# Kernel tuning notes

Measured on AMD Instinct MI355X. Metric: run time of the kernel, lower is better.

## Reference

```python
import jax, jax.numpy as jnp
import numpy as np

B, S, HID, H, D = 2, 2048, 2048, 16, 128
ROPE_THETA = 10000.0
NEG = -1e9


def _rope_tables(seq_len, dim, theta):
    inv_freq = 1.0 / (theta ** (jnp.arange(0, dim, 2, dtype=jnp.float32) / dim))
    t = jnp.arange(seq_len, dtype=jnp.float32)
    freqs = jnp.outer(t, inv_freq)                 # [S, D/2]
    emb = jnp.concatenate([freqs, freqs], axis=-1)  # [S, D]
    return jnp.cos(emb), jnp.sin(emb)


def _rotate_half(x):
    x1, x2 = jnp.split(x, 2, axis=-1)
    return jnp.concatenate([-x2, x1], axis=-1)


def setup_inputs() -> dict:
    key = jax.random.key(0)
    ks = jax.random.split(key, 12)
    hidden_states = jax.random.normal(ks[0], (B, S, HID), dtype=jnp.float32)
    Wq = jax.random.normal(ks[1], (HID, HID), dtype=jnp.float32) * 0.02
    Wk = jax.random.normal(ks[2], (HID, HID), dtype=jnp.float32) * 0.02
    Wv = jax.random.normal(ks[3], (HID, HID), dtype=jnp.float32) * 0.02
    Wo = jax.random.normal(ks[4], (HID, HID), dtype=jnp.float32) * 0.02
    bq = jnp.zeros((HID,), jnp.float32)
    bk = jnp.zeros((HID,), jnp.float32)
    bv = jnp.zeros((HID,), jnp.float32)
    beta = jax.random.normal(ks[5], (1,), dtype=jnp.float32)
    M = jax.random.normal(ks[6], (H, D, D), dtype=jnp.float32) * 0.01
    z = jax.random.uniform(ks[7], (H, D), dtype=jnp.float32) + 1.0  # strictly positive normalizer
    causal = jnp.tril(jnp.ones((S, S), dtype=bool))
    attention_mask = jnp.broadcast_to(
        jnp.where(causal, 0.0, NEG).astype(jnp.float32)[None, None], (B, 1, S, S)
    ) + jnp.zeros((B, 1, S, S), jnp.float32)
    position_ids = jnp.broadcast_to(jnp.arange(S, dtype=jnp.int32), (B, S))
    return {
        "hidden_states": hidden_states, "Wq": Wq, "bq": bq, "Wk": Wk, "bk": bk,
        "Wv": Wv, "bv": bv, "Wo": Wo, "beta": beta, "M": M, "z": z,
        "attention_mask": attention_mask, "position_ids": position_ids,
    }


def reference(hidden_states, Wq, bq, Wk, bk, Wv, bv, Wo, beta, M, z,
              attention_mask, position_ids):
    bsz, seq, hid = hidden_states.shape
    h, d = M.shape[0], M.shape[1]

    # projections (weights stored [in, out])
    q = (hidden_states @ Wq + bq).reshape(bsz, seq, h, d).transpose(0, 2, 1, 3)  # [b,h,s,d]
    k = (hidden_states @ Wk + bk).reshape(bsz, seq, h, d).transpose(0, 2, 1, 3)
    v = (hidden_states @ Wv + bv).reshape(bsz, seq, h, d).transpose(0, 2, 1, 3)

    # RoPE
    cos, sin = _rope_tables(seq, d, ROPE_THETA)          # [s, d]
    cos = cos[position_ids][:, None]                      # [b,1,s,d]
    sin = sin[position_ids][:, None]
    q = q * cos + _rotate_half(q) * sin
    k = k * cos + _rotate_half(k) * sin

    sigma = lambda x: jax.nn.elu(x) + 1.0
    sig_q = sigma(q)
    sig_k = sigma(k)

    # compressive-memory retrieval (uses pre-update M, z)
    mem_num = jnp.einsum('bhsd,hde->bhse', sig_q, M)
    mem_den = jnp.einsum('bhsd,hd->bhs', sig_q, z)
    memory_output = mem_num / mem_den[..., None]

    # memory update via outer products of feature-mapped keys and values
    M_new = M + jnp.einsum('bhsd,bhse->hde', sig_k, v)
    z_new = z + sig_k.sum(axis=(0, 2))

    # local causal attention
    scores = jnp.einsum('bhqd,bhkd->bhqk', q, k) / jnp.sqrt(jnp.float32(d))
    scores = scores + attention_mask
    attn = jax.nn.softmax(scores, axis=-1)
    attn_output = jnp.einsum('bhqk,bhkd->bhqd', attn, v)

    # gated long-term injection
    g = jax.nn.sigmoid(beta)[0]
    combined = g * memory_output + (1.0 - g) * attn_output

    combined = combined.transpose(0, 2, 1, 3).reshape(bsz, seq, h * d)
    final_output = combined @ Wo
    return (final_output, M_new, z_new)
```

## Files before the change

### kernel.cpp

```cpp
#include <hip/hip_runtime.h>


typedef float  floatx4 __attribute__((ext_vector_type(4)));
typedef __bf16 bf16x8  __attribute__((ext_vector_type(8)));

#define DEV __device__ __forceinline__

constexpr int BN  = 2;
constexpr int SS  = 2048;
constexpr int HID = 2048;
constexpr int NH  = 16;
constexpr int DD  = 128;
constexpr int BS  = BN * SS;

DEV unsigned short f2bf(float f) {
  unsigned int u = __float_as_uint(f);
  u += 0x7FFFu + ((u >> 16) & 1u);
  return (unsigned short)(u >> 16);
}
DEV float bf2f(unsigned short h) {
  return __uint_as_float(((unsigned int)h) << 16);
}
DEV float sigma_f(float x) { return x > 0.f ? x + 1.f : __expf(x); }

DEV void cp16(const unsigned short* g, unsigned short* l) {
  __builtin_amdgcn_global_load_lds(
      (const __attribute__((address_space(1))) unsigned int*)g,
      (__attribute__((address_space(3))) unsigned int*)l, 16, 0, 0);
}

DEV bf16x8 scale8(bf16x8 x, float s) {
  bf16x8 r;
  #pragma unroll
  for (int i = 0; i < 8; i++) r[i] = (__bf16)((float)x[i] * s);
  return r;
}

constexpr size_t WS_WOT   = 0;
constexpr size_t WS_HSB   = WS_WOT   + (size_t)HID * HID * 2;
constexpr size_t WS_WQT   = WS_HSB   + (size_t)BS  * HID * 2;
constexpr size_t WS_WKT   = WS_WQT   + (size_t)HID * HID * 2;
constexpr size_t WS_WVT   = WS_WKT   + (size_t)HID * HID * 2;
constexpr size_t WS_QB    = WS_WVT   + (size_t)HID * HID * 2;
constexpr size_t WS_KB    = WS_QB    + (size_t)BS  * HID * 2;
constexpr size_t WS_VB    = WS_KB    + (size_t)BS  * HID * 2;
constexpr size_t WS_VTB   = WS_VB    + (size_t)BS  * HID * 2;
constexpr size_t WS_ATT   = WS_VTB   + (size_t)BS  * HID * 2;
constexpr size_t WS_COMB  = WS_ATT   + (size_t)BS  * HID * 2;
constexpr size_t WS_MPART = WS_COMB  + (size_t)BS  * HID * 2;
constexpr size_t WS_ZPART = WS_MPART + (size_t)16 * NH * DD * DD * 4;

__global__ __launch_bounds__(256) void k_prep(const float* __restrict__ hs,
                                              const float* __restrict__ Wq, const float* __restrict__ Wk,
                                              const float* __restrict__ Wv, const float* __restrict__ Wo,
                                              unsigned short* __restrict__ hsb,
                                              unsigned short* tq, unsigned short* tk,
                                              unsigned short* tv, unsigned short* to_) {
  __shared__ float tile[64][65];
  const int tid = threadIdx.x;
  if (blockIdx.z == 4) {
    int cid = blockIdx.y * 32 + blockIdx.x;
    const float4* src = (const float4*)hs;
    ushort4* dst = (ushort4*)hsb;
    #pragma unroll
    for (int i = 0; i < 8; i++) {
      int idx = cid * 2048 + i * 256 + tid;
      float4 v = src[idx];
      ushort4 o; o.x = f2bf(v.x); o.y = f2bf(v.y); o.z = f2bf(v.z); o.w = f2bf(v.w);
      dst[idx] = o;
    }
    return;
  }
  const float* W; unsigned short* T;
  switch (blockIdx.z) {
    case 0:  W = Wq; T = tq; break;
    case 1:  W = Wk; T = tk; break;
    case 2:  W = Wv; T = tv; break;
    default: W = Wo; T = to_; break;
  }
  int k0 = blockIdx.y * 64, n0 = blockIdx.x * 64;
  #pragma unroll
  for (int i = 0; i < 16; i++) {
    int idx = i * 256 + tid; int r = idx >> 6, c = idx & 63;
    tile[r][c] = W[(size_t)(k0 + r) * HID + n0 + c];
  }
  __syncthreads();
  #pragma unroll
  for (int i = 0; i < 16; i++) {
    int idx = i * 256 + tid; int r = idx >> 6, c = idx & 63;
    T[(size_t)(n0 + r) * HID + k0 + c] = f2bf(tile[c][r]);
  }
}

constexpr int GBM = 256, GBN = 128, GBK = 64;
constexpr int NTK = HID / GBK;
constexpr int SLOT_U = (GBM + GBN) * GBK;
constexpr int A_U    = GBM * GBK;

DEV void stage_tile(const unsigned short* __restrict__ X,
                    const unsigned short* __restrict__ Wt,
                    unsigned short* slot, int m0, int n0, int k0, int tid) {
  #pragma unroll
  for (int i = 0; i < 4; i++) {
    int c = i * 512 + tid;
    int row = c >> 3;
    int col = k0 + (((c & 7) ^ (row & 7)) << 3);
    cp16(X + (size_t)(m0 + row) * HID + col, slot + c * 8);
  }
  #pragma unroll
  for (int i = 0; i < 2; i++) {
    int c = i * 512 + tid;
    int row = c >> 3;
    int col = k0 + (((c & 7) ^ (row & 7)) << 3);
    cp16(Wt + (size_t)(n0 + row) * HID + col, slot + A_U + c * 8);
  }
}

DEV void gemm_core(const unsigned short* __restrict__ X,
                   const unsigned short* __restrict__ Wt,
                   unsigned short* lds, int m0, int n0, floatx4 acc[4][4]) {
  const int tid = threadIdx.x;
  const int lane = tid & 63, w = tid >> 6;
  const int grp = lane >> 4, l16 = lane & 15;
  const int wm = (w >> 1) * 64, wn = (w & 1) * 64;
  const int swz = (l16 & 7) << 3;
  #pragma unroll
  for (int i = 0; i < 4; i++)
    #pragma unroll
    for (int j = 0; j < 4; j++) acc[i][j] = floatx4{0.f, 0.f, 0.f, 0.f};
  stage_tile(X, Wt, lds,          m0, n0, 0,   tid);
  stage_tile(X, Wt, lds + SLOT_U, m0, n0, GBK, tid);
  int sl_r = 0, sl_w = 2;
  for (int t = 0; t < NTK; t++) {
    if (t + 1 < NTK) asm volatile("s_waitcnt vmcnt(6)" ::: "memory");
    else             asm volatile("s_waitcnt vmcnt(0)" ::: "memory");
    __builtin_amdgcn_s_barrier();
    asm volatile("" ::: "memory");
    if (t + 2 < NTK)
      stage_tile(X, Wt, lds + sl_w * SLOT_U, m0, n0, (t + 2) * GBK, tid);
    const unsigned short* As = lds + sl_r * SLOT_U;
    const unsigned short* Bs = As + A_U;
    bf16x8 af[4][2], bfr[4][2];
    #pragma unroll
    for (int mi = 0; mi < 4; mi++)
      #pragma unroll
      for (int ks = 0; ks < 2; ks++)
        af[mi][ks] = __builtin_bit_cast(bf16x8,
            *(const uint4*)(As + (wm + mi * 16 + l16) * 64 + ((ks * 32 + grp * 8) ^ swz)));
    #pragma unroll
    for (int ni = 0; ni < 4; ni++)
      #pragma unroll
      for (int ks = 0; ks < 2; ks++)
        bfr[ni][ks] = __builtin_bit_cast(bf16x8,
            *(const uint4*)(Bs + (wn + ni * 16 + l16) * 64 + ((ks * 32 + grp * 8) ^ swz)));
    __builtin_amdgcn_s_setprio(1);
    #pragma unroll
    for (int mi = 0; mi < 4; mi++)
      #pragma unroll
      for (int ni = 0; ni < 4; ni++)
        #pragma unroll
        for (int ks = 0; ks < 2; ks++)
          acc[mi][ni] = __builtin_amdgcn_mfma_f32_16x16x32_bf16(af[mi][ks], bfr[ni][ks], acc[mi][ni], 0, 0, 0);
    __builtin_amdgcn_s_setprio(0);
    asm volatile("" ::: "memory");
    sl_r = (sl_r == 2) ? 0 : sl_r + 1;
    sl_w = (sl_w == 2) ? 0 : sl_w + 1;
  }
}

__global__ __launch_bounds__(512, 2) void k_gemm_qkv(
    const unsigned short* __restrict__ Xb,
    const unsigned short* __restrict__ Wtq, const unsigned short* __restrict__ Wtk,
    const unsigned short* __restrict__ Wtv,
    const float* __restrict__ bq, const float* __restrict__ bk, const float* __restrict__ bv,
    unsigned short* __restrict__ qb, unsigned short* __restrict__ kb,
    unsigned short* __restrict__ vb, unsigned short* __restrict__ vtb) {
  const unsigned short* Wt; const float* bias; unsigned short* out;
  switch (blockIdx.z) {
    case 0:  Wt = Wtq; bias = bq; out = qb; break;
    case 1:  Wt = Wtk; bias = bk; out = kb; break;
    default: Wt = Wtv; bias = bv; out = vb; break;
  }
  __shared__ __align__(16) unsigned short lds[3 * SLOT_U];
  int lin = blockIdx.y * 16 + blockIdx.x;
  lin = (lin & 7) * 32 + (lin >> 3);
  int m0 = (lin >> 4) * GBM, n0 = (lin & 15) * GBN;
  floatx4 acc[4][4];
  gemm_core(Xb, Wt, lds, m0, n0, acc);
  const int lane = threadIdx.x & 63, w = threadIdx.x >> 6;
  const int grp = lane >> 4, l16 = lane & 15;
  const int wm = (w >> 1) * 64, wn = (w & 1) * 64;
  const bool isv = (blockIdx.z == 2);
  #pragma unroll
  for (int mi = 0; mi < 4; mi++) {
    int gr0 = m0 + wm + mi * 16;
    int bi  = gr0 >> 11;
    int ssb = (gr0 & 2047) + grp * 4;
    #pragma unroll
    for (int ni = 0; ni < 4; ni++) {
      int col = n0 + wn + ni * 16 + l16;
      float bb_ = bias[col];
      int hh = col >> 7, dd = col & 127;
      ushort4 pk;
      unsigned short* pv = (unsigned short*)&pk;
      #pragma unroll
      for (int r = 0; r < 4; r++) {
        unsigned short val = f2bf(acc[mi][ni][r] + bb_);
        out[(((size_t)(bi * NH + hh)) * SS + ssb + r) * DD + dd] = val;
        pv[r] = val;
      }
      if (isv)
        *(ushort4*)(vtb + (((size_t)(bi * NH + hh)) * DD + dd) * SS + ssb) = pk;
    }
  }
}

__global__ __launch_bounds__(512, 2) void k_gemm_out(const unsigned short* __restrict__ Xb,
                                                     const unsigned short* __restrict__ Wt,
                                                     float* __restrict__ outf) {
  __shared__ __align__(16) unsigned short lds[3 * SLOT_U];
  int lin = blockIdx.y * 16 + blockIdx.x;
  lin = (lin & 7) * 32 + (lin >> 3);
  int m0 = (lin >> 4) * GBM, n0 = (lin & 15) * GBN;
  floatx4 acc[4][4];
  gemm_core(Xb, Wt, lds, m0, n0, acc);
  const int lane = threadIdx.x & 63, w = threadIdx.x >> 6;
  const int grp = lane >> 4, l16 = lane & 15;
  const int wm = (w >> 1) * 64, wn = (w & 1) * 64;
  #pragma unroll
  for (int mi = 0; mi < 4; mi++)
    #pragma unroll
    for (int ni = 0; ni < 4; ni++) {
      int col = n0 + wn + ni * 16 + l16;
      #pragma unroll
      for (int r = 0; r < 4; r++) {
        int gr = m0 + wm + mi * 16 + grp * 4 + r;
        outf[(size_t)gr * HID + col] = acc[mi][ni][r];
      }
    }
}

__global__ __launch_bounds__(256) void k_rope(unsigned short* __restrict__ qb,
                                              unsigned short* __restrict__ kb) {
  int row = blockIdx.x * 4 + (threadIdx.x >> 6);
  int d = threadIdx.x & 63;
  int s = row & (SS - 1);
  size_t base = (size_t)row * DD;
  float ang = (float)s * __expf(-(float)d * (9.210340371976184f / 64.f));
  float sn, c;
  __sincosf(ang, &sn, &c);
  float q1 = bf2f(qb[base + d]), q2 = bf2f(qb[base + d + 64]);
  qb[base + d]      = f2bf(q1 * c - q2 * sn);
  qb[base + d + 64] = f2bf(q2 * c + q1 * sn);
  float k1 = bf2f(kb[base + d]), k2 = bf2f(kb[base + d + 64]);
  kb[base + d]      = f2bf(k1 * c - k2 * sn);
  kb[base + d + 64] = f2bf(k2 * c + k1 * sn);
}

DEV void stage_kv(const unsigned short* __restrict__ Kg,
                  const unsigned short* __restrict__ Vg,
                  unsigned short* Klb, unsigned short* Vtlb, int tid) {
  #pragma unroll
  for (int i = 0; i < 4; i++) {
    int c = i * 256 + tid;
    int kv = c >> 4, ck = c & 15;
    cp16(Kg + kv * DD + ((ck ^ (kv & 7)) << 3), Klb + c * 8);
    int dvt = c >> 3, cv = c & 7;
    cp16(Vg + (size_t)dvt * SS + ((cv ^ (dvt & 7)) << 3), Vtlb + c * 8);
  }
}

DEV void attn_update(const unsigned short* Kl, const unsigned short* Vtl,
                     unsigned short* Plw, const bf16x8* qf, floatx4* o,
                     floatx4* lacc, bool diag, int grp, int l16, int wrow) {
  const int swk = l16 & 7;
  floatx4 sacc[4];
  #pragma unroll
  for (int j = 0; j < 4; j++) sacc[j] = floatx4{0.f, 0.f, 0.f, 0.f};
  __builtin_amdgcn_s_setprio(1);
  #pragma unroll
  for (int ks = 0; ks < 4; ks++)
    #pragma unroll
    for (int j = 0; j < 4; j++) {
      bf16x8 kf = __builtin_bit_cast(bf16x8,
          *(const uint4*)(Kl + (j * 16 + l16) * 128 + (((ks * 4 + grp) ^ swk) << 3)));
      sacc[j] = __builtin_amdgcn_mfma_f32_16x16x32_bf16(qf[ks], kf, sacc[j], 0, 0, 0);
    }
  __builtin_amdgcn_s_setprio(0);
  #pragma unroll
  for (int j = 0; j < 4; j++)
    #pragma unroll
    for (int r = 0; r < 4; r++) {
      float p = (diag && (j * 16 + l16) > (wrow + grp * 4 + r)) ? 0.f : __expf(sacc[j][r]);
      Plw[(j >> 1) * 640 + (grp * 4 + r) * 40 + (j & 1) * 16 + l16] = f2bf(p);
    }
  const bf16x8 ones = __builtin_bit_cast(bf16x8,
      uint4{0x3F803F80u, 0x3F803F80u, 0x3F803F80u, 0x3F803F80u});
  __builtin_amdgcn_s_setprio(1);
  #pragma unroll
  for (int ks2 = 0; ks2 < 2; ks2++) {
    bf16x8 pf = __builtin_bit_cast(bf16x8,
        *(const uint4*)(Plw + ks2 * 640 + l16 * 40 + grp * 8));
    *lacc = __builtin_amdgcn_mfma_f32_16x16x32_bf16(pf, ones, *lacc, 0, 0, 0);
    #pragma unroll
    for (int n = 0; n < 8; n++) {
      bf16x8 vf = __builtin_bit_cast(bf16x8,
          *(const uint4*)(Vtl + (n * 16 + l16) * 64 + (((ks2 * 4 + grp) ^ swk) << 3)));
      o[n] = __builtin_amdgcn_mfma_f32_16x16x32_bf16(pf, vf, o[n], 0, 0, 0);
    }
  }
  __builtin_amdgcn_s_setprio(0);
}

__global__ __launch_bounds__(256) void k_attn(const unsigned short* __restrict__ qb,
                                              const unsigned short* __restrict__ kb,
                                              const unsigned short* __restrict__ vtb,
                                              unsigned short* __restrict__ attb) {
  const int t = blockIdx.x, bh = blockIdx.y;
  const int qtA = t, qtB = 31 - t;
  const int tid = threadIdx.x, w = tid >> 6, lane = tid & 63;
  const int grp = lane >> 4, l16 = lane & 15;
  const unsigned short* Q  = qb  + (size_t)bh * SS * DD;
  const unsigned short* K  = kb  + (size_t)bh * SS * DD;
  const unsigned short* VT = vtb + (size_t)bh * DD * SS;
  __shared__ __align__(16) unsigned short Kl[2][64 * 128];
  __shared__ __align__(16) unsigned short Vtl[2][128 * 64];
  __shared__ __align__(16) unsigned short Pl[4][1280];
  const float sc = 0.08838834764831845f;
  bf16x8 qfA[4], qfB[4];
  {
    int qrA = qtA * 64 + w * 16 + l16, qrB = qtB * 64 + w * 16 + l16;
    #pragma unroll
    for (int ks = 0; ks < 4; ks++) {
      qfA[ks] = scale8(__builtin_bit_cast(bf16x8, *(const uint4*)(Q + (size_t)qrA * DD + ks * 32 + grp * 8)), sc);
      qfB[ks] = scale8(__builtin_bit_cast(bf16x8, *(const uint4*)(Q + (size_t)qrB * DD + ks * 32 + grp * 8)), sc);
    }
  }
  floatx4 oA[8], oB[8];
  #pragma unroll
  for (int n = 0; n < 8; n++) { oA[n] = floatx4{0,0,0,0}; oB[n] = floatx4{0,0,0,0}; }
  floatx4 laccA = floatx4{0,0,0,0}, laccB = floatx4{0,0,0,0};
  stage_kv(K, VT, Kl[0], Vtl[0], tid);
  asm volatile("s_waitcnt vmcnt(0)" ::: "memory");
  __builtin_amdgcn_s_barrier();
  int cur = 0;
  for (int kt = 0; kt <= qtB; kt++) {
    asm volatile("" ::: "memory");
    if (kt < qtB)
      stage_kv(K + (size_t)(kt + 1) * 64 * DD, VT + (size_t)(kt + 1) * 64,
               Kl[cur ^ 1], Vtl[cur ^ 1], tid);
    attn_update(Kl[cur], Vtl[cur], Pl[w], qfB, oB, &laccB, kt == qtB, grp, l16, w * 16);
    if (kt <= qtA)
      attn_update(Kl[cur], Vtl[cur], Pl[w], qfA, oA, &laccA, kt == qtA, grp, l16, w * 16);
    asm volatile("" ::: "memory");
    if (kt < qtB) {
      asm volatile("s_waitcnt vmcnt(0)" ::: "memory");
      __builtin_amdgcn_s_barrier();
    }
    cur ^= 1;
  }
  #pragma unroll
  for (int r = 0; r < 4; r++) {
    float invA = 1.f / laccA[r], invB = 1.f / laccB[r];
    int rA = qtA * 64 + w * 16 + grp * 4 + r;
    int rB = qtB * 64 + w * 16 + grp * 4 + r;
    #pragma unroll
    for (int n = 0; n < 8; n++) {
      attb[(size_t)bh * SS * DD + (size_t)rA * DD + n * 16 + l16] = f2bf(oA[n][r] * invA);
      attb[(size_t)bh * SS * DD + (size_t)rB * DD + n * 16 + l16] = f2bf(oB[n][r] * invB);
    }
  }
}

__global__ __launch_bounds__(256) void k_memcomb(const unsigned short* __restrict__ qb,
                                                 const float* __restrict__ M,
                                                 const float* __restrict__ z,
                                                 const float* __restrict__ beta,
                                                 const unsigned short* __restrict__ attb,
                                                 unsigned short* __restrict__ comb) {
  const int st = blockIdx.x, bh = blockIdx.y;
  const int b = bh >> 4, h = bh & 15;
  const int tid = threadIdx.x;
  const int te = tid & 31, ts = tid >> 5;
  const int s0 = st * 64;
  __shared__ float Ml[16][128];
  __shared__ float sq[64][16];
  __shared__ float zl[16];
  float acc[8][4]; float den[8];
  #pragma unroll
  for (int i = 0; i < 8; i++) { den[i] = 0.f; for (int j = 0; j < 4; j++) acc[i][j] = 0.f; }
  const float* Mh = M + (size_t)h * DD * DD;
  for (int dc = 0; dc < DD; dc += 16) {
    __syncthreads();
    #pragma unroll
    for (int i = 0; i < 8; i++) {
      int idx = i * 256 + tid; int r = idx >> 7, cc = idx & 127;
      Ml[r][cc] = Mh[(size_t)(dc + r) * DD + cc];
    }
    #pragma unroll
    for (int i = 0; i < 4; i++) {
      int idx = i * 256 + tid; int r = idx >> 4, cc = idx & 15;
      sq[r][cc] = sigma_f(bf2f(qb[((size_t)bh * SS + s0 + r) * DD + dc + cc]));
    }
    if (tid < 16) zl[tid] = z[h * DD + dc + tid];
    __syncthreads();
    for (int dd = 0; dd < 16; dd++) {
      float zv = zl[dd];
      float m0_ = Ml[dd][te * 4 + 0], m1_ = Ml[dd][te * 4 + 1];
      float m2_ = Ml[dd][te * 4 + 2], m3_ = Ml[dd][te * 4 + 3];
      #pragma unroll
      for (int si = 0; si < 8; si++) {
        float sv = sq[ts * 8 + si][dd];
        den[si] += sv * zv;
        acc[si][0] += sv * m0_; acc[si][1] += sv * m1_;
        acc[si][2] += sv * m2_; acc[si][3] += sv * m3_;
      }
    }
  }
  float g = 1.f / (1.f + __expf(-beta[0]));
  #pragma unroll
  for (int si = 0; si < 8; si++) {
    int s = s0 + ts * 8 + si;
    float dinv = 1.f / den[si];
    #pragma unroll
    for (int ei = 0; ei < 4; ei++) {
      float mo = acc[si][ei] * dinv;
      float at = bf2f(attb[((size_t)bh * SS + s) * DD + te * 4 + ei]);
      float cvv = g * mo + (1.f - g) * at;
      comb[((size_t)(b * SS + s)) * HID + h * DD + te * 4 + ei] = f2bf(cvv);
    }
  }
}

__global__ __launch_bounds__(256) void k_mnew(const unsigned short* __restrict__ kb,
                                              const unsigned short* __restrict__ vb,
                                              float* __restrict__ mpart,
                                              float* __restrict__ zpart) {
  const int ch = blockIdx.x, h = blockIdx.y;
  const int tid = threadIdx.x;
  const int td = tid >> 4, te = tid & 15;
  __shared__ float sk[16][128], vv[16][128];
  float acc[8][8];
  float zacc = 0.f;
  #pragma unroll
  for (int a = 0; a < 8; a++)
    #pragma unroll
    for (int b2 = 0; b2 < 8; b2++) acc[a][b2] = 0.f;
  for (int c0 = 0; c0 < 256; c0 += 16) {
    __syncthreads();
    #pragma unroll
    for (int i = 0; i < 8; i++) {
      int idx = i * 256 + tid; int r = idx >> 7, cc = idx & 127;
      int bs = ch * 256 + c0 + r;
      size_t addr = ((size_t)((bs >> 11) * NH + h) * SS + (bs & 2047)) * DD + cc;
      float skv = sigma_f(bf2f(kb[addr]));
      sk[r][cc] = skv;
      zacc += skv;
      vv[r][cc] = bf2f(vb[addr]);
    }
    __syncthreads();
    for (int i = 0; i < 16; i++) {
      float ks_[8], vs_[8];
      #pragma unroll
      for (int a = 0; a < 8; a++) ks_[a] = sk[i][td * 8 + a];
      #pragma unroll
      for (int b2 = 0; b2 < 8; b2++) vs_[b2] = vv[i][te * 8 + b2];
      #pragma unroll
      for (int a = 0; a < 8; a++)
        #pragma unroll
        for (int b2 = 0; b2 < 8; b2++) acc[a][b2] += ks_[a] * vs_[b2];
    }
  }
  float* mp = mpart + ((size_t)ch * NH + h) * DD * DD;
  #pragma unroll
  for (int a = 0; a < 8; a++)
    #pragma unroll
    for (int b2 = 0; b2 < 8; b2++)
      mp[(size_t)(td * 8 + a) * DD + te * 8 + b2] = acc[a][b2];
  __syncthreads();
  float* red = (float*)sk;
  red[tid] = zacc;
  __syncthreads();
  if (tid < 128)
    zpart[((size_t)ch * NH + h) * DD + tid] = red[tid] + red[tid + 128];
}

__global__ __launch_bounds__(256) void k_mreduce(const float* __restrict__ M,
                                                 const float* __restrict__ mpart,
                                                 const float* __restrict__ z,
                                                 const float* __restrict__ zpart,
                                                 float* __restrict__ outM,
                                                 float* __restrict__ outz) {
  int idx = blockIdx.x * 256 + threadIdx.x;
  float s = M[idx];
  #pragma unroll
  for (int ch = 0; ch < 16; ch++) s += mpart[(size_t)ch * NH * DD * DD + idx];
  outM[idx] = s;
  if (blockIdx.x < 8) {
    int zi = blockIdx.x * 256 + threadIdx.x;
    float zs = z[zi];
    #pragma unroll
    for (int ch = 0; ch < 16; ch++) zs += zpart[(size_t)ch * NH * DD + zi];
    outz[zi] = zs;
  }
}

extern "C" void kernel_launch(void* const* d_in, const int* in_sizes, int n_in,
                              void* d_out, int out_size, void* d_ws, size_t ws_size,
                              hipStream_t stream) {
  const float* hs   = (const float*)d_in[0];
  const float* Wq   = (const float*)d_in[1];
  const float* bq   = (const float*)d_in[2];
  const float* Wk   = (const float*)d_in[3];
  const float* bk   = (const float*)d_in[4];
  const float* Wv   = (const float*)d_in[5];
  const float* bv   = (const float*)d_in[6];
  const float* Wo   = (const float*)d_in[7];
  const float* beta = (const float*)d_in[8];
  const float* M    = (const float*)d_in[9];
  const float* z    = (const float*)d_in[10];

  char* ws = (char*)d_ws;
  unsigned short* wot  = (unsigned short*)(ws + WS_WOT);
  unsigned short* hsb  = (unsigned short*)(ws + WS_HSB);
  unsigned short* wqt  = (unsigned short*)(ws + WS_WQT);
  unsigned short* wkt  = (unsigned short*)(ws + WS_WKT);
  unsigned short* wvt  = (unsigned short*)(ws + WS_WVT);
  unsigned short* qb   = (unsigned short*)(ws + WS_QB);
  unsigned short* kb   = (unsigned short*)(ws + WS_KB);
  unsigned short* vb   = (unsigned short*)(ws + WS_VB);
  unsigned short* vtb  = (unsigned short*)(ws + WS_VTB);
  unsigned short* attb = (unsigned short*)(ws + WS_ATT);
  unsigned short* comb = (unsigned short*)(ws + WS_COMB);
  float*          mprt = (float*)(ws + WS_MPART);
  float*          zprt = (float*)(ws + WS_ZPART);

  float* out_final = (float*)d_out;
  float* out_M = out_final + (size_t)BS * HID;
  float* out_z = out_M + NH * DD * DD;

  k_prep    <<<dim3(32, 32, 5),        256, 0, stream>>>(hs, Wq, Wk, Wv, Wo, hsb, wqt, wkt, wvt, wot);
  k_gemm_qkv<<<dim3(16, 16, 3),        512, 0, stream>>>(hsb, wqt, wkt, wvt, bq, bk, bv, qb, kb, vb, vtb);
  k_rope    <<<dim3(BN * NH * SS / 4), 256, 0, stream>>>(qb, kb);
  k_attn    <<<dim3(16, 32),           256, 0, stream>>>(qb, kb, vtb, attb);
  k_memcomb <<<dim3(32, 32),           256, 0, stream>>>(qb, M, z, beta, attb, comb);
  k_gemm_out<<<dim3(16, 16),           512, 0, stream>>>(comb, wot, out_final);
  k_mnew    <<<dim3(16, 16),           256, 0, stream>>>(kb, vb, mprt, zprt);
  k_mreduce <<<dim3(1024),             256, 0, stream>>>(M, mprt, z, zprt, out_M, out_z);
}
```

Before: 532.7 us.

## Split GEMM k-step into four interleaved LDS-load/MFMA phases with staggered prefetch

The GEMM inner iteration is restructured into four quadrant phases. Each phase loads part of the A/B fragments from LDS, issues part of the next tile's global-to-LDS copies, then runs a 2x2 block of MFMAs, with extra workgroup barriers between phases. The goal is to overlap LDS reads and global prefetch with matrix-core work, similar to ping-pong scheduling, and to reduce register pressure from holding all fragments at once. In exchange it adds several barriers per k-step, which could stall waves.

```diff
diff --git a/kernel.cpp b/kernel.cpp
--- a/kernel.cpp
+++ b/kernel.cpp
@@ -34,6 +34,10 @@
   #pragma unroll
   for (int i = 0; i < 8; i++) r[i] = (__bf16)((float)x[i] * s);
   return r;
+}
+
+DEV floatx4 mfma16(bf16x8 a, bf16x8 b, floatx4 c) {
+  return __builtin_amdgcn_mfma_f32_16x16x32_bf16(a, b, c, 0, 0, 0);
 }
 
 constexpr size_t WS_WOT   = 0;
@@ -97,24 +101,33 @@
 constexpr int SLOT_U = (GBM + GBN) * GBK;
 constexpr int A_U    = GBM * GBK;
 
+DEV void stage_a1(const unsigned short* __restrict__ X,
+                  unsigned short* slot, int m0, int k0, int tid, int i) {
+  int c = i * 512 + tid;
+  int row = c >> 3;
+  int col = k0 + (((c & 7) ^ (row & 7)) << 3);
+  cp16(X + (size_t)(m0 + row) * HID + col, slot + c * 8);
+}
+DEV void stage_b1(const unsigned short* __restrict__ Wt,
+                  unsigned short* slot, int n0, int k0, int tid, int i) {
+  int c = i * 512 + tid;
+  int row = c >> 3;
+  int col = k0 + (((c & 7) ^ (row & 7)) << 3);
+  cp16(Wt + (size_t)(n0 + row) * HID + col, slot + A_U + c * 8);
+}
 DEV void stage_tile(const unsigned short* __restrict__ X,
                     const unsigned short* __restrict__ Wt,
                     unsigned short* slot, int m0, int n0, int k0, int tid) {
   #pragma unroll
-  for (int i = 0; i < 4; i++) {
-    int c = i * 512 + tid;
-    int row = c >> 3;
-    int col = k0 + (((c & 7) ^ (row & 7)) << 3);
-    cp16(X + (size_t)(m0 + row) * HID + col, slot + c * 8);
-  }
-  #pragma unroll
-  for (int i = 0; i < 2; i++) {
-    int c = i * 512 + tid;
-    int row = c >> 3;
-    int col = k0 + (((c & 7) ^ (row & 7)) << 3);
-    cp16(Wt + (size_t)(n0 + row) * HID + col, slot + A_U + c * 8);
-  }
-}
+  for (int i = 0; i < 4; i++) stage_a1(X, slot, m0, k0, tid, i);
+  #pragma unroll
+  for (int i = 0; i < 2; i++) stage_b1(Wt, slot, n0, k0, tid, i);
+}
+
+#define LDA(mi, ks) __builtin_bit_cast(bf16x8, \
+    *(const uint4*)(As + (wm + (mi) * 16 + l16) * 64 + (((ks) * 32 + grp * 8) ^ swz)))
+#define LDB(ni, ks) __builtin_bit_cast(bf16x8, \
+    *(const uint4*)(Bs + (wn + (ni) * 16 + l16) * 64 + (((ks) * 32 + grp * 8) ^ swz)))
 
 DEV void gemm_core(const unsigned short* __restrict__ X,
                    const unsigned short* __restrict__ Wt,
@@ -136,37 +149,79 @@
     else             asm volatile("s_waitcnt vmcnt(0)" ::: "memory");
     __builtin_amdgcn_s_barrier();
     asm volatile("" ::: "memory");
-    if (t + 2 < NTK)
-      stage_tile(X, Wt, lds + sl_w * SLOT_U, m0, n0, (t + 2) * GBK, tid);
     const unsigned short* As = lds + sl_r * SLOT_U;
     const unsigned short* Bs = As + A_U;
-    bf16x8 af[4][2], bfr[4][2];
-    #pragma unroll
-    for (int mi = 0; mi < 4; mi++)
-      #pragma unroll
-      for (int ks = 0; ks < 2; ks++)
-        af[mi][ks] = __builtin_bit_cast(bf16x8,
-            *(const uint4*)(As + (wm + mi * 16 + l16) * 64 + ((ks * 32 + grp * 8) ^ swz)));
-    #pragma unroll
-    for (int ni = 0; ni < 4; ni++)
-      #pragma unroll
-      for (int ks = 0; ks < 2; ks++)
-        bfr[ni][ks] = __builtin_bit_cast(bf16x8,
-            *(const uint4*)(Bs + (wn + ni * 16 + l16) * 64 + ((ks * 32 + grp * 8) ^ swz)));
+    const bool pf = (t + 2 < NTK);
+    unsigned short* wslot = lds + sl_w * SLOT_U;
+    const int k2 = (t + 2) * GBK;
+    bf16x8 afA[2][2], afB[2][2], bfA[2][2], bfB[2][2];
+    #pragma unroll
+    for (int ks = 0; ks < 2; ks++) {
+      afA[0][ks] = LDA(0, ks); afA[1][ks] = LDA(1, ks);
+      bfA[0][ks] = LDB(0, ks); bfA[1][ks] = LDB(1, ks);
+    }
+    if (pf) { stage_a1(X, wslot, m0, k2, tid, 0); stage_a1(X, wslot, m0, k2, tid, 1); }
+    __builtin_amdgcn_s_barrier();
+    asm volatile("s_waitcnt lgkmcnt(0)" ::: "memory");
+    __builtin_amdgcn_sched_barrier(0);
     __builtin_amdgcn_s_setprio(1);
     #pragma unroll
-    for (int mi = 0; mi < 4; mi++)
-      #pragma unroll
-      for (int ni = 0; ni < 4; ni++)
-        #pragma unroll
-        for (int ks = 0; ks < 2; ks++)
-          acc[mi][ni] = __builtin_amdgcn_mfma_f32_16x16x32_bf16(af[mi][ks], bfr[ni][ks], acc[mi][ni], 0, 0, 0);
+    for (int ks = 0; ks < 2; ks++) {
+      acc[0][0] = mfma16(afA[0][ks], bfA[0][ks], acc[0][0]);
+      acc[0][1] = mfma16(afA[0][ks], bfA[1][ks], acc[0][1]);
+      acc[1][0] = mfma16(afA[1][ks], bfA[0][ks], acc[1][0]);
+      acc[1][1] = mfma16(afA[1][ks], bfA[1][ks], acc[1][1]);
+    }
+    __builtin_amdgcn_s_setprio(0);
+    __builtin_amdgcn_s_barrier();
+    #pragma unroll
+    for (int ks = 0; ks < 2; ks++) { bfB[0][ks] = LDB(2, ks); bfB[1][ks] = LDB(3, ks); }
+    if (pf) { stage_a1(X, wslot, m0, k2, tid, 2); stage_a1(X, wslot, m0, k2, tid, 3); }
+    __builtin_amdgcn_s_barrier();
+    asm volatile("s_waitcnt lgkmcnt(0)" ::: "memory");
+    __builtin_amdgcn_sched_barrier(0);
+    __builtin_amdgcn_s_setprio(1);
+    #pragma unroll
+    for (int ks = 0; ks < 2; ks++) {
+      acc[0][2] = mfma16(afA[0][ks], bfB[0][ks], acc[0][2]);
+      acc[0][3] = mfma16(afA[0][ks], bfB[1][ks], acc[0][3]);
+      acc[1][2] = mfma16(afA[1][ks], bfB[0][ks], acc[1][2]);
+      acc[1][3] = mfma16(afA[1][ks], bfB[1][ks], acc[1][3]);
+    }
+    __builtin_amdgcn_s_setprio(0);
+    __builtin_amdgcn_s_barrier();
+    #pragma unroll
+    for (int ks = 0; ks < 2; ks++) { afB[0][ks] = LDA(2, ks); afB[1][ks] = LDA(3, ks); }
+    if (pf) { stage_b1(Wt, wslot, n0, k2, tid, 0); stage_b1(Wt, wslot, n0, k2, tid, 1); }
+    __builtin_amdgcn_s_barrier();
+    asm volatile("s_waitcnt lgkmcnt(0)" ::: "memory");
+    __builtin_amdgcn_sched_barrier(0);
+    __builtin_amdgcn_s_setprio(1);
+    #pragma unroll
+    for (int ks = 0; ks < 2; ks++) {
+      acc[2][2] = mfma16(afB[0][ks], bfB[0][ks], acc[2][2]);
+      acc[2][3] = mfma16(afB[0][ks], bfB[1][ks], acc[2][3]);
+      acc[3][2] = mfma16(afB[1][ks], bfB[0][ks], acc[3][2]);
+      acc[3][3] = mfma16(afB[1][ks], bfB[1][ks], acc[3][3]);
+    }
+    __builtin_amdgcn_s_setprio(0);
+    __builtin_amdgcn_s_barrier();
+    __builtin_amdgcn_s_setprio(1);
+    #pragma unroll
+    for (int ks = 0; ks < 2; ks++) {
+      acc[2][0] = mfma16(afB[0][ks], bfA[0][ks], acc[2][0]);
+      acc[2][1] = mfma16(afB[0][ks], bfA[1][ks], acc[2][1]);
+      acc[3][0] = mfma16(afB[1][ks], bfA[0][ks], acc[3][0]);
+      acc[3][1] = mfma16(afB[1][ks], bfA[1][ks], acc[3][1]);
+    }
     __builtin_amdgcn_s_setprio(0);
     asm volatile("" ::: "memory");
     sl_r = (sl_r == 2) ? 0 : sl_r + 1;
     sl_w = (sl_w == 2) ? 0 : sl_w + 1;
   }
 }
+#undef LDA
+#undef LDB
 
 __global__ __launch_bounds__(512, 2) void k_gemm_qkv(
     const unsigned short* __restrict__ Xb,
```

Result: faster. 517.2 us (-2.9%).

## Enlarge GEMM tiles to 256x256 with phased double-buffered MFMA schedule

Applied to the files above, without the earlier changes.

The shared bf16 GEMM core moves from 256x128 to 256x256 block tiles. Each wave now owns a 128x64 sub-tile, which doubles per-wave register reuse of A and B fragments. The triple-buffered prefetch is replaced by a double buffer, and each K step is split into four barrier-separated MFMA phases, with fragment loads and global-to-LDS prefetches interleaved between them. Block-index remapping is updated for the new grid sizes. In exchange, LDS use grows to about 128 KB per block, which likely allows only one block per CU. The output GEMM launches just 128 blocks, which may leave many CUs idle.

```diff
diff --git a/kernel.cpp b/kernel.cpp
--- a/kernel.cpp
+++ b/kernel.cpp
@@ -34,6 +34,10 @@
   #pragma unroll
   for (int i = 0; i < 8; i++) r[i] = (__bf16)((float)x[i] * s);
   return r;
+}
+
+DEV floatx4 mfma16(bf16x8 a, bf16x8 b, floatx4 c) {
+  return __builtin_amdgcn_mfma_f32_16x16x32_bf16(a, b, c, 0, 0, 0);
 }
 
 constexpr size_t WS_WOT   = 0;
@@ -92,79 +96,122 @@
   }
 }
 
-constexpr int GBM = 256, GBN = 128, GBK = 64;
+constexpr int GBM = 256, GBN = 256, GBK = 64;
 constexpr int NTK = HID / GBK;
+constexpr int A_U    = GBM * GBK;
 constexpr int SLOT_U = (GBM + GBN) * GBK;
-constexpr int A_U    = GBM * GBK;
-
-DEV void stage_tile(const unsigned short* __restrict__ X,
-                    const unsigned short* __restrict__ Wt,
-                    unsigned short* slot, int m0, int n0, int k0, int tid) {
-  #pragma unroll
-  for (int i = 0; i < 4; i++) {
-    int c = i * 512 + tid;
-    int row = c >> 3;
-    int col = k0 + (((c & 7) ^ (row & 7)) << 3);
-    cp16(X + (size_t)(m0 + row) * HID + col, slot + c * 8);
-  }
-  #pragma unroll
-  for (int i = 0; i < 2; i++) {
-    int c = i * 512 + tid;
-    int row = c >> 3;
-    int col = k0 + (((c & 7) ^ (row & 7)) << 3);
-    cp16(Wt + (size_t)(n0 + row) * HID + col, slot + A_U + c * 8);
-  }
+
+DEV void stage_q(const unsigned short* __restrict__ X,
+                 const unsigned short* __restrict__ Wt,
+                 unsigned short* slot, int m0, int n0, int k0, int tid, int q) {
+  int c = q * 512 + tid;
+  int row = c >> 3;
+  int col = k0 + (((c & 7) ^ (row & 7)) << 3);
+  cp16(X  + (size_t)(m0 + row) * HID + col, slot + c * 8);
+  cp16(Wt + (size_t)(n0 + row) * HID + col, slot + A_U + c * 8);
+}
+
+DEV bf16x8 ldf(const unsigned short* base, int row, int kofs) {
+  return __builtin_bit_cast(bf16x8, *(const uint4*)(base + row * 64 + kofs));
 }
 
 DEV void gemm_core(const unsigned short* __restrict__ X,
                    const unsigned short* __restrict__ Wt,
-                   unsigned short* lds, int m0, int n0, floatx4 acc[4][4]) {
+                   unsigned short* lds, int m0, int n0, floatx4 acc[8][4]) {
   const int tid = threadIdx.x;
   const int lane = tid & 63, w = tid >> 6;
   const int grp = lane >> 4, l16 = lane & 15;
-  const int wm = (w >> 1) * 64, wn = (w & 1) * 64;
-  const int swz = (l16 & 7) << 3;
-  #pragma unroll
-  for (int i = 0; i < 4; i++)
+  const int wm = (w >> 2) * 128, wn = (w & 3) * 64;
+  const int swz  = (l16 & 7) << 3;
+  const int kof0 = (grp * 8) ^ swz;
+  const int kof1 = (32 + grp * 8) ^ swz;
+  #pragma unroll
+  for (int i = 0; i < 8; i++)
     #pragma unroll
     for (int j = 0; j < 4; j++) acc[i][j] = floatx4{0.f, 0.f, 0.f, 0.f};
-  stage_tile(X, Wt, lds,          m0, n0, 0,   tid);
-  stage_tile(X, Wt, lds + SLOT_U, m0, n0, GBK, tid);
-  int sl_r = 0, sl_w = 2;
+  #pragma unroll
+  for (int q = 0; q < 4; q++) stage_q(X, Wt, lds, m0, n0, 0, tid, q);
   for (int t = 0; t < NTK; t++) {
-    if (t + 1 < NTK) asm volatile("s_waitcnt vmcnt(6)" ::: "memory");
-    else             asm volatile("s_waitcnt vmcnt(0)" ::: "memory");
+    const unsigned short* As = lds + (t & 1) * SLOT_U;
+    const unsigned short* Bs = As + A_U;
+    unsigned short* wslot = lds + ((t + 1) & 1) * SLOT_U;
+    const int k1 = (t + 1) * GBK;
+    const bool pf = (t + 1 < NTK);
+    asm volatile("s_waitcnt vmcnt(0)" ::: "memory");
     __builtin_amdgcn_s_barrier();
     asm volatile("" ::: "memory");
-    if (t + 2 < NTK)
-      stage_tile(X, Wt, lds + sl_w * SLOT_U, m0, n0, (t + 2) * GBK, tid);
-    const unsigned short* As = lds + sl_r * SLOT_U;
-    const unsigned short* Bs = As + A_U;
-    bf16x8 af[4][2], bfr[4][2];
+    bf16x8 afL[4][2], afH[4][2], bfL[2][2], bfH[2][2];
+    #pragma unroll
+    for (int mi = 0; mi < 4; mi++) {
+      afL[mi][0] = ldf(As, wm + mi * 16 + l16, kof0);
+      afL[mi][1] = ldf(As, wm + mi * 16 + l16, kof1);
+    }
+    #pragma unroll
+    for (int ni = 0; ni < 2; ni++) {
+      bfL[ni][0] = ldf(Bs, wn + ni * 16 + l16, kof0);
+      bfL[ni][1] = ldf(Bs, wn + ni * 16 + l16, kof1);
+    }
+    if (pf) { stage_q(X, Wt, wslot, m0, n0, k1, tid, 0); stage_q(X, Wt, wslot, m0, n0, k1, tid, 1); }
+    __builtin_amdgcn_s_barrier();
+    asm volatile("s_waitcnt lgkmcnt(0)" ::: "memory");
+    __builtin_amdgcn_sched_barrier(0);
+    __builtin_amdgcn_s_setprio(1);
     #pragma unroll
     for (int mi = 0; mi < 4; mi++)
       #pragma unroll
-      for (int ks = 0; ks < 2; ks++)
-        af[mi][ks] = __builtin_bit_cast(bf16x8,
-            *(const uint4*)(As + (wm + mi * 16 + l16) * 64 + ((ks * 32 + grp * 8) ^ swz)));
-    #pragma unroll
-    for (int ni = 0; ni < 4; ni++)
-      #pragma unroll
-      for (int ks = 0; ks < 2; ks++)
-        bfr[ni][ks] = __builtin_bit_cast(bf16x8,
-            *(const uint4*)(Bs + (wn + ni * 16 + l16) * 64 + ((ks * 32 + grp * 8) ^ swz)));
-    __builtin_amdgcn_s_setprio(1);
-    #pragma unroll
-    for (int mi = 0; mi < 4; mi++)
-      #pragma unroll
-      for (int ni = 0; ni < 4; ni++)
+      for (int ni = 0; ni < 2; ni++)
         #pragma unroll
         for (int ks = 0; ks < 2; ks++)
-          acc[mi][ni] = __builtin_amdgcn_mfma_f32_16x16x32_bf16(af[mi][ks], bfr[ni][ks], acc[mi][ni], 0, 0, 0);
+          acc[mi][ni] = mfma16(afL[mi][ks], bfL[ni][ks], acc[mi][ni]);
+    __builtin_amdgcn_s_setprio(0);
+    __builtin_amdgcn_s_barrier();
+    #pragma unroll
+    for (int ni = 0; ni < 2; ni++) {
+      bfH[ni][0] = ldf(Bs, wn + (ni + 2) * 16 + l16, kof0);
+      bfH[ni][1] = ldf(Bs, wn + (ni + 2) * 16 + l16, kof1);
+    }
+    if (pf) { stage_q(X, Wt, wslot, m0, n0, k1, tid, 2); stage_q(X, Wt, wslot, m0, n0, k1, tid, 3); }
+    __builtin_amdgcn_s_barrier();
+    asm volatile("s_waitcnt lgkmcnt(0)" ::: "memory");
+    __builtin_amdgcn_sched_barrier(0);
+    __builtin_amdgcn_s_setprio(1);
+    #pragma unroll
+    for (int mi = 0; mi < 4; mi++)
+      #pragma unroll
+      for (int ni = 0; ni < 2; ni++)
+        #pragma unroll
+        for (int ks = 0; ks < 2; ks++)
+          acc[mi][ni + 2] = mfma16(afL[mi][ks], bfH[ni][ks], acc[mi][ni + 2]);
+    __builtin_amdgcn_s_setprio(0);
+    __builtin_amdgcn_s_barrier();
+    #pragma unroll
+    for (int mi = 0; mi < 4; mi++) {
+      afH[mi][0] = ldf(As, wm + (mi + 4) * 16 + l16, kof0);
+      afH[mi][1] = ldf(As, wm + (mi + 4) * 16 + l16, kof1);
+    }
+    __builtin_amdgcn_s_barrier();
+    asm volatile("s_waitcnt lgkmcnt(0)" ::: "memory");
+    __builtin_amdgcn_sched_barrier(0);
+    __builtin_amdgcn_s_setprio(1);
+    #pragma unroll
+    for (int mi = 0; mi < 4; mi++)
+      #pragma unroll
+      for (int ni = 0; ni < 2; ni++)
+        #pragma unroll
+        for (int ks = 0; ks < 2; ks++)
+          acc[mi + 4][ni + 2] = mfma16(afH[mi][ks], bfH[ni][ks], acc[mi + 4][ni + 2]);
+    __builtin_amdgcn_s_setprio(0);
+    __builtin_amdgcn_s_barrier();
+    __builtin_amdgcn_s_setprio(1);
+    #pragma unroll
+    for (int mi = 0; mi < 4; mi++)
+      #pragma unroll
+      for (int ni = 0; ni < 2; ni++)
+        #pragma unroll
+        for (int ks = 0; ks < 2; ks++)
+          acc[mi + 4][ni] = mfma16(afH[mi][ks], bfL[ni][ks], acc[mi + 4][ni]);
     __builtin_amdgcn_s_setprio(0);
     asm volatile("" ::: "memory");
-    sl_r = (sl_r == 2) ? 0 : sl_r + 1;
-    sl_w = (sl_w == 2) ? 0 : sl_w + 1;
   }
 }
 
@@ -175,24 +222,25 @@
     const float* __restrict__ bq, const float* __restrict__ bk, const float* __restrict__ bv,
     unsigned short* __restrict__ qb, unsigned short* __restrict__ kb,
     unsigned short* __restrict__ vb, unsigned short* __restrict__ vtb) {
+  __shared__ __align__(16) unsigned short lds[2 * SLOT_U];
+  int o = blockIdx.z * 128 + blockIdx.y * 8 + blockIdx.x;
+  int s = (o & 7) * 48 + (o >> 3);
+  int zz = s >> 7, rem = s & 127;
+  int m0 = (rem >> 3) * GBM, n0 = (rem & 7) * GBN;
   const unsigned short* Wt; const float* bias; unsigned short* out;
-  switch (blockIdx.z) {
+  switch (zz) {
     case 0:  Wt = Wtq; bias = bq; out = qb; break;
     case 1:  Wt = Wtk; bias = bk; out = kb; break;
     default: Wt = Wtv; bias = bv; out = vb; break;
   }
-  __shared__ __align__(16) unsigned short lds[3 * SLOT_U];
-  int lin = blockIdx.y * 16 + blockIdx.x;
-  lin = (lin & 7) * 32 + (lin >> 3);
-  int m0 = (lin >> 4) * GBM, n0 = (lin & 15) * GBN;
-  floatx4 acc[4][4];
+  floatx4 acc[8][4];
   gemm_core(Xb, Wt, lds, m0, n0, acc);
   const int lane = threadIdx.x & 63, w = threadIdx.x >> 6;
   const int grp = lane >> 4, l16 = lane & 15;
-  const int wm = (w >> 1) * 64, wn = (w & 1) * 64;
-  const bool isv = (blockIdx.z == 2);
-  #pragma unroll
-  for (int mi = 0; mi < 4; mi++) {
+  const int wm = (w >> 2) * 128, wn = (w & 3) * 64;
+  const bool isv = (zz == 2);
+  #pragma unroll
+  for (int mi = 0; mi < 8; mi++) {
     int gr0 = m0 + wm + mi * 16;
     int bi  = gr0 >> 11;
     int ssb = (gr0 & 2047) + grp * 4;
@@ -218,17 +266,17 @@
 __global__ __launch_bounds__(512, 2) void k_gemm_out(const unsigned short* __restrict__ Xb,
                                                      const unsigned short* __restrict__ Wt,
                                                      float* __restrict__ outf) {
-  __shared__ __align__(16) unsigned short lds[3 * SLOT_U];
-  int lin = blockIdx.y * 16 + blockIdx.x;
-  lin = (lin & 7) * 32 + (lin >> 3);
-  int m0 = (lin >> 4) * GBM, n0 = (lin & 15) * GBN;
-  floatx4 acc[4][4];
+  __shared__ __align__(16) unsigned short lds[2 * SLOT_U];
+  int o = blockIdx.y * 8 + blockIdx.x;
+  int s = (o & 7) * 16 + (o >> 3);
+  int m0 = (s >> 3) * GBM, n0 = (s & 7) * GBN;
+  floatx4 acc[8][4];
   gemm_core(Xb, Wt, lds, m0, n0, acc);
   const int lane = threadIdx.x & 63, w = threadIdx.x >> 6;
   const int grp = lane >> 4, l16 = lane & 15;
-  const int wm = (w >> 1) * 64, wn = (w & 1) * 64;
-  #pragma unroll
-  for (int mi = 0; mi < 4; mi++)
+  const int wm = (w >> 2) * 128, wn = (w & 3) * 64;
+  #pragma unroll
+  for (int mi = 0; mi < 8; mi++)
     #pragma unroll
     for (int ni = 0; ni < 4; ni++) {
       int col = n0 + wn + ni * 16 + l16;
@@ -540,11 +588,11 @@
   float* out_z = out_M + NH * DD * DD;
 
   k_prep    <<<dim3(32, 32, 5),        256, 0, stream>>>(hs, Wq, Wk, Wv, Wo, hsb, wqt, wkt, wvt, wot);
-  k_gemm_qkv<<<dim3(16, 16, 3),        512, 0, stream>>>(hsb, wqt, wkt, wvt, bq, bk, bv, qb, kb, vb, vtb);
+  k_gemm_qkv<<<dim3(8, 16, 3),         512, 0, stream>>>(hsb, wqt, wkt, wvt, bq, bk, bv, qb, kb, vb, vtb);
   k_rope    <<<dim3(BN * NH * SS / 4), 256, 0, stream>>>(qb, kb);
   k_attn    <<<dim3(16, 32),           256, 0, stream>>>(qb, kb, vtb, attb);
   k_memcomb <<<dim3(32, 32),           256, 0, stream>>>(qb, M, z, beta, attb, comb);
-  k_gemm_out<<<dim3(16, 16),           512, 0, stream>>>(comb, wot, out_final);
+  k_gemm_out<<<dim3(8, 16),            512, 0, stream>>>(comb, wot, out_final);
   k_mnew    <<<dim3(16, 16),           256, 0, stream>>>(kb, vb, mprt, zprt);
   k_mreduce <<<dim3(1024),             256, 0, stream>>>(M, mprt, z, zprt, out_M, out_z);
 }
```

New measurement: 555.1 us. 1.04x slower.

## Halve GEMM K-tile to 32 with new LDS swizzle to raise occupancy

Applied to the files above, without the earlier changes.

Shrinks the GEMM K-step from 64 to 32, halving the triple-buffered LDS footprint and the fragment registers per thread, and raises the launch-bounds occupancy hint from 2 to 4 blocks per CU. A new swizzle packs two 32-element rows per 64-element LDS line to avoid bank conflicts, and the waitcnt is adjusted to the smaller per-stage load count. The aim is more resident waves to hide latency, at the cost of twice as many barriers and loop iterations and possible register spilling under the tighter bound.

```diff
diff --git a/kernel.cpp b/kernel.cpp
--- a/kernel.cpp
+++ b/kernel.cpp
@@ -34,6 +34,10 @@
   #pragma unroll
   for (int i = 0; i < 8; i++) r[i] = (__bf16)((float)x[i] * s);
   return r;
+}
+
+DEV floatx4 mfma16(bf16x8 a, bf16x8 b, floatx4 c) {
+  return __builtin_amdgcn_mfma_f32_16x16x32_bf16(a, b, c, 0, 0, 0);
 }
 
 constexpr size_t WS_WOT   = 0;
@@ -92,28 +96,33 @@
   }
 }
 
-constexpr int GBM = 256, GBN = 128, GBK = 64;
+constexpr int GBM = 256, GBN = 128, GBK = 32;
 constexpr int NTK = HID / GBK;
+constexpr int A_U    = GBM * GBK;
 constexpr int SLOT_U = (GBM + GBN) * GBK;
-constexpr int A_U    = GBM * GBK;
-
-DEV void stage_tile(const unsigned short* __restrict__ X,
+
+DEV void stage_slot(const unsigned short* __restrict__ X,
                     const unsigned short* __restrict__ Wt,
                     unsigned short* slot, int m0, int n0, int k0, int tid) {
   #pragma unroll
-  for (int i = 0; i < 4; i++) {
-    int c = i * 512 + tid;
-    int row = c >> 3;
-    int col = k0 + (((c & 7) ^ (row & 7)) << 3);
-    cp16(X + (size_t)(m0 + row) * HID + col, slot + c * 8);
-  }
-  #pragma unroll
   for (int i = 0; i < 2; i++) {
     int c = i * 512 + tid;
-    int row = c >> 3;
-    int col = k0 + (((c & 7) ^ (row & 7)) << 3);
+    int q = c >> 3, p = c & 7, t = p ^ (q & 7);
+    int row = 2 * q + (t >> 2), col = k0 + ((t & 3) << 3);
+    cp16(X + (size_t)(m0 + row) * HID + col, slot + c * 8);
+  }
+  {
+    int c = tid;
+    int q = c >> 3, p = c & 7, t = p ^ (q & 7);
+    int row = 2 * q + (t >> 2), col = k0 + ((t & 3) << 3);
     cp16(Wt + (size_t)(n0 + row) * HID + col, slot + A_U + c * 8);
   }
+}
+
+DEV bf16x8 ldfrag(const unsigned short* base, int r, int grp) {
+  int q = r >> 1;
+  int p = (((r & 1) << 2) | grp) ^ (q & 7);
+  return __builtin_bit_cast(bf16x8, *(const uint4*)(base + q * 64 + p * 8));
 }
 
 DEV void gemm_core(const unsigned short* __restrict__ X,
@@ -123,44 +132,33 @@
   const int lane = tid & 63, w = tid >> 6;
   const int grp = lane >> 4, l16 = lane & 15;
   const int wm = (w >> 1) * 64, wn = (w & 1) * 64;
-  const int swz = (l16 & 7) << 3;
   #pragma unroll
   for (int i = 0; i < 4; i++)
     #pragma unroll
     for (int j = 0; j < 4; j++) acc[i][j] = floatx4{0.f, 0.f, 0.f, 0.f};
-  stage_tile(X, Wt, lds,          m0, n0, 0,   tid);
-  stage_tile(X, Wt, lds + SLOT_U, m0, n0, GBK, tid);
+  stage_slot(X, Wt, lds,          m0, n0, 0,   tid);
+  stage_slot(X, Wt, lds + SLOT_U, m0, n0, GBK, tid);
   int sl_r = 0, sl_w = 2;
   for (int t = 0; t < NTK; t++) {
-    if (t + 1 < NTK) asm volatile("s_waitcnt vmcnt(6)" ::: "memory");
+    if (t + 1 < NTK) asm volatile("s_waitcnt vmcnt(3)" ::: "memory");
     else             asm volatile("s_waitcnt vmcnt(0)" ::: "memory");
     __builtin_amdgcn_s_barrier();
     asm volatile("" ::: "memory");
     if (t + 2 < NTK)
-      stage_tile(X, Wt, lds + sl_w * SLOT_U, m0, n0, (t + 2) * GBK, tid);
+      stage_slot(X, Wt, lds + sl_w * SLOT_U, m0, n0, (t + 2) * GBK, tid);
     const unsigned short* As = lds + sl_r * SLOT_U;
     const unsigned short* Bs = As + A_U;
-    bf16x8 af[4][2], bfr[4][2];
+    bf16x8 af[4], bfr[4];
+    #pragma unroll
+    for (int mi = 0; mi < 4; mi++) af[mi]  = ldfrag(As, wm + mi * 16 + l16, grp);
+    #pragma unroll
+    for (int ni = 0; ni < 4; ni++) bfr[ni] = ldfrag(Bs, wn + ni * 16 + l16, grp);
+    __builtin_amdgcn_s_setprio(1);
     #pragma unroll
     for (int mi = 0; mi < 4; mi++)
       #pragma unroll
-      for (int ks = 0; ks < 2; ks++)
-        af[mi][ks] = __builtin_bit_cast(bf16x8,
-            *(const uint4*)(As + (wm + mi * 16 + l16) * 64 + ((ks * 32 + grp * 8) ^ swz)));
-    #pragma unroll
-    for (int ni = 0; ni < 4; ni++)
-      #pragma unroll
-      for (int ks = 0; ks < 2; ks++)
-        bfr[ni][ks] = __builtin_bit_cast(bf16x8,
-            *(const uint4*)(Bs + (wn + ni * 16 + l16) * 64 + ((ks * 32 + grp * 8) ^ swz)));
-    __builtin_amdgcn_s_setprio(1);
-    #pragma unroll
-    for (int mi = 0; mi < 4; mi++)
-      #pragma unroll
       for (int ni = 0; ni < 4; ni++)
-        #pragma unroll
-        for (int ks = 0; ks < 2; ks++)
-          acc[mi][ni] = __builtin_amdgcn_mfma_f32_16x16x32_bf16(af[mi][ks], bfr[ni][ks], acc[mi][ni], 0, 0, 0);
+        acc[mi][ni] = mfma16(af[mi], bfr[ni], acc[mi][ni]);
     __builtin_amdgcn_s_setprio(0);
     asm volatile("" ::: "memory");
     sl_r = (sl_r == 2) ? 0 : sl_r + 1;
@@ -168,7 +166,7 @@
   }
 }
 
-__global__ __launch_bounds__(512, 2) void k_gemm_qkv(
+__global__ __launch_bounds__(512, 4) void k_gemm_qkv(
     const unsigned short* __restrict__ Xb,
     const unsigned short* __restrict__ Wtq, const unsigned short* __restrict__ Wtk,
     const unsigned short* __restrict__ Wtv,
@@ -215,7 +213,7 @@
   }
 }
 
-__global__ __launch_bounds__(512, 2) void k_gemm_out(const unsigned short* __restrict__ Xb,
+__global__ __launch_bounds__(512, 4) void k_gemm_out(const unsigned short* __restrict__ Xb,
                                                      const unsigned short* __restrict__ Wt,
                                                      float* __restrict__ outf) {
   __shared__ __align__(16) unsigned short lds[3 * SLOT_U];
```

Result: no change. 536.8 us (+0.8%).
